# Performance work log

Measured on AMD Instinct MI355X. Metric: run time of the kernel, lower is better.

Reference implementation:

```python
import jax, jax.numpy as jnp
import numpy as np

N_NODES = 500_000
N_EDGES = 16_000_000


def setup_inputs() -> dict:
    key = jax.random.key(0)
    ks = jax.random.split(key, 10)
    x = jax.random.normal(ks[0], (N_NODES, 8), dtype=jnp.float32)
    edge_index = jax.random.randint(ks[1], (2, N_EDGES), 0, N_NODES, dtype=jnp.int64)
    W1_l = jax.random.normal(ks[2], (8, 32), dtype=jnp.float32) * 0.1
    W1_r = jax.random.normal(ks[3], (8, 32), dtype=jnp.float32) * 0.1
    b1 = jax.random.normal(ks[4], (32,), dtype=jnp.float32) * 0.1
    W2_l = jax.random.normal(ks[5], (32, 16), dtype=jnp.float32) * 0.1
    W2_r = jax.random.normal(ks[6], (32, 16), dtype=jnp.float32) * 0.1
    b2 = jax.random.normal(ks[7], (16,), dtype=jnp.float32) * 0.1
    W_out = jax.random.normal(ks[8], (16, 1), dtype=jnp.float32) * 0.1
    b_out = jax.random.normal(ks[9], (1,), dtype=jnp.float32) * 0.1
    return {"x": x, "edge_index": edge_index, "W1_l": W1_l, "W1_r": W1_r, "b1": b1,
            "W2_l": W2_l, "W2_r": W2_r, "b2": b2, "W_out": W_out, "b_out": b_out}


def _sage_conv(x, src, dst, deg_inv, W_l, W_r, b):
    # mean-aggregate neighbor features: gather x[src], scatter-add to dst, divide by degree
    agg = jax.ops.segment_sum(x[src], dst, num_segments=N_NODES)  # [N, d_in]
    mean_nb = agg * deg_inv[:, None]
    return mean_nb @ W_l + x @ W_r + b


def reference(x, edge_index, W1_l, W1_r, b1, W2_l, W2_r, b2, W_out, b_out):
    src, dst = edge_index[0], edge_index[1]
    # in-degree per target node (mean aggregation denominator), clamped at 1
    deg = jax.ops.segment_sum(jnp.ones((src.shape[0],), dtype=x.dtype), dst,
                              num_segments=N_NODES)
    deg_inv = 1.0 / jnp.maximum(deg, 1.0)
    h = jax.nn.relu(_sage_conv(x, src, dst, deg_inv, W1_l, W1_r, b1))
    # dropout(p=0.1) is identity at inference
    h = jax.nn.relu(_sage_conv(h, src, dst, deg_inv, W2_l, W2_r, b2))
    return jax.nn.sigmoid(h @ W_out + b_out)  # [N, 1]
```

## Files before the change

kernel.cpp:

```cpp
#include <hip/hip_runtime.h>
#include <hip/hip_fp16.h>
#include <math.h>

#define N_NODES 500000
#define N_EDGES 16000000

#define NBUCKET 2048
#define NPB 256
#define NSB 64
#define NSLICE 32
#define NB_USED 1954
#define BUCKET_CAP 9216

#define NCH_H 500
#define CHUNK_H 32000
#define NCH_A 1000
#define CHUNK_A 16000

#define OFF_TOT     0
#define OFF_BASE    8192
#define OFF_FCUR    16512
#define OFF_SBCUR   24704
#define OFF_AUXB    24960
#define OFF_ROW     25600
#define OFF_DEG     2025600
#define OFF_XH8     4025600
#define OFF_PAIRS   8025664
#define OFF_AUX     72025664
#define OFF_H1P8    72025664
#define OFF_S2      80025664

typedef float v2f __attribute__((ext_vector_type(2)));

static __device__ inline float2 up2(unsigned int u) {
  __half2 h = *reinterpret_cast<__half2*>(&u);
  return __half22float2(h);
}
static __device__ inline unsigned int ph2(float a, float b) {
  __half2 h = __floats2half2_rn(a, b);
  return *reinterpret_cast<unsigned int*>(&h);
}
static __device__ inline unsigned int pk_fp8x4(float a, float b, float c, float d) {
  int u = __builtin_amdgcn_cvt_pk_fp8_f32(a, b, 0, false);
  u = __builtin_amdgcn_cvt_pk_fp8_f32(c, d, u, true);
  return (unsigned int)u;
}
static __device__ inline void acc8(float* a, uint2 g) {
  v2f f01 = __builtin_amdgcn_cvt_pk_f32_fp8((int)g.x, false);
  v2f f23 = __builtin_amdgcn_cvt_pk_f32_fp8((int)g.x, true);
  v2f f45 = __builtin_amdgcn_cvt_pk_f32_fp8((int)g.y, false);
  v2f f67 = __builtin_amdgcn_cvt_pk_f32_fp8((int)g.y, true);
  a[0] += f01.x; a[1] += f01.y; a[2] += f23.x; a[3] += f23.y;
  a[4] += f45.x; a[5] += f45.y; a[6] += f67.x; a[7] += f67.y;
}
static __device__ inline void acc16(float* a, uint4 g) {
  v2f f0 = __builtin_amdgcn_cvt_pk_f32_fp8((int)g.x, false);
  v2f f1 = __builtin_amdgcn_cvt_pk_f32_fp8((int)g.x, true);
  v2f f2 = __builtin_amdgcn_cvt_pk_f32_fp8((int)g.y, false);
  v2f f3 = __builtin_amdgcn_cvt_pk_f32_fp8((int)g.y, true);
  v2f f4 = __builtin_amdgcn_cvt_pk_f32_fp8((int)g.z, false);
  v2f f5 = __builtin_amdgcn_cvt_pk_f32_fp8((int)g.z, true);
  v2f f6 = __builtin_amdgcn_cvt_pk_f32_fp8((int)g.w, false);
  v2f f7 = __builtin_amdgcn_cvt_pk_f32_fp8((int)g.w, true);
  a[0] += f0.x;  a[1] += f0.y;  a[2] += f1.x;  a[3] += f1.y;
  a[4] += f2.x;  a[5] += f2.y;  a[6] += f3.x;  a[7] += f3.y;
  a[8] += f4.x;  a[9] += f4.y;  a[10] += f5.x; a[11] += f5.y;
  a[12] += f6.x; a[13] += f6.y; a[14] += f7.x; a[15] += f7.y;
}

__global__ __launch_bounds__(256) void k_xcast(const float* __restrict__ x,
                                               uint2* __restrict__ xh8) {
  int i = blockIdx.x * 256 + threadIdx.x;
  if (i >= N_NODES) return;
  const float4* xp = (const float4*)(x + (size_t)i * 8);
  float4 a = xp[0], b = xp[1];
  uint2 v;
  v.x = pk_fp8x4(a.x, a.y, a.z, a.w);
  v.y = pk_fp8x4(b.x, b.y, b.z, b.w);
  xh8[i] = v;
}

__global__ __launch_bounds__(256) void k_hist(const int* __restrict__ ei,
                                              int* __restrict__ tot) {
  __shared__ int hist[NBUCKET];
  int t = threadIdx.x;
  int c = blockIdx.x;
#pragma unroll
  for (int j = 0; j < NBUCKET / 256; j++) hist[t + j * 256] = 0;
  __syncthreads();
  int e0 = c * CHUNK_H;
  const int ng = CHUNK_H / 4;
  for (int g = t; g < ng; g += 256) {
    uint4 d4 = *(const uint4*)(ei + N_EDGES + e0 + g * 4);
    atomicAdd(&hist[d4.x >> 8], 1);
    atomicAdd(&hist[d4.y >> 8], 1);
    atomicAdd(&hist[d4.z >> 8], 1);
    atomicAdd(&hist[d4.w >> 8], 1);
  }
  __syncthreads();
#pragma unroll
  for (int j = 0; j < NBUCKET / 256; j++) {
    int b = t + j * 256;
    if (hist[b]) atomicAdd(&tot[b], hist[b]);
  }
}

__global__ __launch_bounds__(256) void k_scan(const int* __restrict__ tot,
                                              int* __restrict__ base,
                                              int* __restrict__ fineCur,
                                              int* __restrict__ sbCur,
                                              int* __restrict__ auxBase) {
  __shared__ int lds[256];
  int t = threadIdx.x;
  int loc[8];
  int s = 0;
#pragma unroll
  for (int j = 0; j < 8; j++) {
    loc[j] = s;
    s += tot[t * 8 + j];
  }
  lds[t] = s;
  __syncthreads();
  for (int off = 1; off < 256; off <<= 1) {
    int v = (t >= off) ? lds[t - off] : 0;
    __syncthreads();
    lds[t] += v;
    __syncthreads();
  }
  int eb = (t > 0) ? lds[t - 1] : 0;
#pragma unroll
  for (int j = 0; j < 8; j++) {
    int idx = t * 8 + j;
    int v = eb + loc[j];
    base[idx] = v;
    fineCur[idx] = v;
  }
  if (t == 255) base[NBUCKET] = lds[255];
  if (t < NSB) {
    int v = (t > 0) ? lds[t * 4 - 1] : 0;
    if (t >= 32) v -= lds[127];
    sbCur[t] = v;
    auxBase[t] = v;
  }
}

__global__ __launch_bounds__(256) void k_passA(const int* __restrict__ ei,
                                               int* __restrict__ sbCur,
                                               unsigned int* __restrict__ aux,
                                               int half) {
  __shared__ int hist[NSB];
  __shared__ int cur[NSB];
  int t = threadIdx.x;
  int c = blockIdx.x;
  if (t < NSB) hist[t] = 0;
  __syncthreads();
  int e0 = c * CHUNK_A;
  const int ng = CHUNK_A / 4;
  for (int g = t; g < ng; g += 256) {
    uint4 d4 = *(const uint4*)(ei + N_EDGES + e0 + g * 4);
    unsigned int dd[4] = {d4.x, d4.y, d4.z, d4.w};
#pragma unroll
    for (int j = 0; j < 4; j++) {
      int sb = (int)(dd[j] >> 13);
      if ((sb >> 5) == half) atomicAdd(&hist[sb], 1);
    }
  }
  __syncthreads();
  if (t < NSB) cur[t] = atomicAdd(&sbCur[t], hist[t]);
  __syncthreads();
  for (int g = t; g < ng; g += 256) {
    uint4 s4 = *(const uint4*)(ei + e0 + g * 4);
    uint4 d4 = *(const uint4*)(ei + N_EDGES + e0 + g * 4);
    unsigned int ss[4] = {s4.x, s4.y, s4.z, s4.w};
    unsigned int dd[4] = {d4.x, d4.y, d4.z, d4.w};
#pragma unroll
    for (int j = 0; j < 4; j++) {
      int sb = (int)(dd[j] >> 13);
      if ((sb >> 5) == half) {
        int pos = atomicAdd(&cur[sb], 1);
        aux[pos] = ss[j] | ((dd[j] & 8191u) << 19);
      }
    }
  }
}

__global__ __launch_bounds__(256) void k_passB(const unsigned int* __restrict__ aux,
                                               const int* __restrict__ base,
                                               const int* __restrict__ auxBase,
                                               int* __restrict__ fineCur,
                                               unsigned int* __restrict__ pairs,
                                               int half) {
  __shared__ int hist[32];
  __shared__ int cur[32];
  int t = threadIdx.x;
  int sbl = blockIdx.x / NSLICE;
  int sl = blockIdx.x % NSLICE;
  int sb = half * 32 + sbl;
  int aStart = auxBase[sb];
  int len = base[(sb + 1) << 5] - base[sb << 5];
  int per = (len + NSLICE - 1) / NSLICE;
  int lo = sl * per;
  int hi = lo + per;
  if (hi > len) hi = len;
  if (t < 32) hist[t] = 0;
  __syncthreads();
  for (int k = lo + t; k < hi; k += 256) {
    unsigned int w = aux[aStart + k];
    atomicAdd(&hist[w >> 27], 1);
  }
  __syncthreads();
  if (t < 32) cur[t] = atomicAdd(&fineCur[(sb << 5) + t], hist[t]);
  __syncthreads();
  for (int k = lo + t; k < hi; k += 256) {
    unsigned int w = aux[aStart + k];
    int pos = atomicAdd(&cur[w >> 27], 1);
    pairs[pos] = w;
  }
}

__global__ __launch_bounds__(256) void k_sort(unsigned int* __restrict__ pairs,
                                              const int* __restrict__ base,
                                              int* __restrict__ row,
                                              int* __restrict__ deg) {
  __shared__ unsigned int sp[BUCKET_CAP];
  __shared__ int hist[NPB];
  __shared__ int lds[NPB];
  __shared__ int cur[NPB];
  int t = threadIdx.x;
  int b = blockIdx.x;
  int e0 = base[b];
  int n = base[b + 1] - e0;
  if (n > BUCKET_CAP) n = BUCKET_CAP;
  for (int k = t; k < n; k += 256) sp[k] = pairs[e0 + k];
  hist[t] = 0;
  __syncthreads();
  for (int k = t; k < n; k += 256) atomicAdd(&hist[(sp[k] >> 19) & 255u], 1);
  __syncthreads();
  int h = hist[t];
  lds[t] = h;
  __syncthreads();
  for (int off = 1; off < 256; off <<= 1) {
    int v = (t >= off) ? lds[t - off] : 0;
    __syncthreads();
    lds[t] += v;
    __syncthreads();
  }
  int start = e0 + lds[t] - h;
  cur[t] = start;
  int i = (b << 8) + t;
  if (i < N_NODES) {
    row[i] = start;
    deg[i] = h;
  }
  __syncthreads();
  for (int k = t; k < n; k += 256) {
    unsigned int p = sp[k];
    int ld = (int)((p >> 19) & 255u);
    int pos = atomicAdd(&cur[ld], 1);
    pairs[pos] = p & 0x7FFFFu;
  }
}

__global__ __launch_bounds__(256) void k_l1(
    const unsigned int* __restrict__ adj, const int* __restrict__ row,
    const int* __restrict__ deg, const uint2* __restrict__ xh8,
    const float* __restrict__ x,
    const float* __restrict__ W1l, const float* __restrict__ W1r,
    const float* __restrict__ b1,
    const float* __restrict__ W2l, const float* __restrict__ W2r,
    uint4* __restrict__ h1p8, unsigned int* __restrict__ s2) {
  __shared__ float sW1l[256], sW1r[256], sb1[32], sW2l[512], sW2r[512];
  int t = threadIdx.x;
  sW1l[t] = W1l[t];
  sW1r[t] = W1r[t];
  sW2l[t] = W2l[t];  sW2l[t + 256] = W2l[t + 256];
  sW2r[t] = W2r[t];  sW2r[t + 256] = W2r[t + 256];
  if (t < 32) sb1[t] = b1[t];
  __syncthreads();

  int i = blockIdx.x * 256 + t;
  if (i >= N_NODES) return;
  int rs = row[i];
  int d = deg[i];

  float acc[8] = {0, 0, 0, 0, 0, 0, 0, 0};
  int j = 0;
  for (; j + 4 <= d; j += 4) {
    int a0 = adj[rs + j + 0];
    int a1 = adj[rs + j + 1];
    int a2 = adj[rs + j + 2];
    int a3 = adj[rs + j + 3];
    uint2 g0 = xh8[a0], g1 = xh8[a1], g2 = xh8[a2], g3 = xh8[a3];
    acc8(acc, g0); acc8(acc, g1); acc8(acc, g2); acc8(acc, g3);
  }
  for (; j < d; j++) {
    uint2 g = xh8[adj[rs + j]];
    acc8(acc, g);
  }

  float dinv = 1.0f / fmaxf((float)d, 1.0f);
  float m[8];
#pragma unroll
  for (int f = 0; f < 8; f++) m[f] = acc[f] * dinv;
  const float4* xp = (const float4*)(x + (size_t)i * 8);
  float4 x0 = xp[0], x1 = xp[1];
  float xv[8] = {x0.x, x0.y, x0.z, x0.w, x1.x, x1.y, x1.z, x1.w};

  float h[32];
#pragma unroll
  for (int jj = 0; jj < 32; jj++) h[jj] = sb1[jj];
#pragma unroll
  for (int k = 0; k < 8; k++) {
#pragma unroll
    for (int jj = 0; jj < 32; jj++) {
      h[jj] = fmaf(m[k], sW1l[k * 32 + jj], h[jj]);
      h[jj] = fmaf(xv[k], sW1r[k * 32 + jj], h[jj]);
    }
  }
#pragma unroll
  for (int jj = 0; jj < 32; jj++) h[jj] = fmaxf(h[jj], 0.0f);

  float p[16], s[16];
#pragma unroll
  for (int jj = 0; jj < 16; jj++) { p[jj] = 0.0f; s[jj] = 0.0f; }
#pragma unroll
  for (int k = 0; k < 32; k++) {
#pragma unroll
    for (int jj = 0; jj < 16; jj++) {
      p[jj] = fmaf(h[k], sW2l[k * 16 + jj], p[jj]);
      s[jj] = fmaf(h[k], sW2r[k * 16 + jj], s[jj]);
    }
  }
  uint4 hv;
  hv.x = pk_fp8x4(p[0], p[1], p[2], p[3]);
  hv.y = pk_fp8x4(p[4], p[5], p[6], p[7]);
  hv.z = pk_fp8x4(p[8], p[9], p[10], p[11]);
  hv.w = pk_fp8x4(p[12], p[13], p[14], p[15]);
  h1p8[i] = hv;
  uint4* sp = (uint4*)(s2 + (size_t)i * 8);
  sp[0] = make_uint4(ph2(s[0], s[1]), ph2(s[2], s[3]), ph2(s[4], s[5]), ph2(s[6], s[7]));
  sp[1] = make_uint4(ph2(s[8], s[9]), ph2(s[10], s[11]), ph2(s[12], s[13]), ph2(s[14], s[15]));
}

__global__ __launch_bounds__(256) void k_l2(
    const unsigned int* __restrict__ adj, const int* __restrict__ row,
    const int* __restrict__ deg, const uint4* __restrict__ h1p8,
    const unsigned int* __restrict__ s2, const float* __restrict__ b2,
    const float* __restrict__ Wout, const float* __restrict__ bout,
    float* __restrict__ out) {
  __shared__ float sb2[16], sWo[16], sbo;
  int t = threadIdx.x;
  if (t < 16) { sb2[t] = b2[t]; sWo[t] = Wout[t]; }
  if (t == 0) sbo = bout[0];
  __syncthreads();

  int i = blockIdx.x * 256 + t;
  if (i >= N_NODES) return;
  int rs = row[i];
  int d = deg[i];

  float acc[16];
#pragma unroll
  for (int jj = 0; jj < 16; jj++) acc[jj] = 0.0f;
  int j = 0;
  for (; j + 4 <= d; j += 4) {
    int a0 = adj[rs + j + 0];
    int a1 = adj[rs + j + 1];
    int a2 = adj[rs + j + 2];
    int a3 = adj[rs + j + 3];
    uint4 g0 = h1p8[a0], g1 = h1p8[a1], g2 = h1p8[a2], g3 = h1p8[a3];
    acc16(acc, g0); acc16(acc, g1); acc16(acc, g2); acc16(acc, g3);
  }
  for (; j < d; j++) {
    uint4 g = h1p8[adj[rs + j]];
    acc16(acc, g);
  }

  float dinv = 1.0f / fmaxf((float)d, 1.0f);
  const uint4* sp = (const uint4*)(s2 + (size_t)i * 8);
  uint4 q0 = sp[0], q1 = sp[1];
  float2 s0 = up2(q0.x), s1 = up2(q0.y), s2v = up2(q0.z), s3 = up2(q0.w);
  float2 s4 = up2(q1.x), s5 = up2(q1.y), s6 = up2(q1.z), s7 = up2(q1.w);
  float sv[16] = {s0.x, s0.y, s1.x, s1.y, s2v.x, s2v.y, s3.x, s3.y,
                  s4.x, s4.y, s5.x, s5.y, s6.x, s6.y, s7.x, s7.y};
  float o = sbo;
#pragma unroll
  for (int c = 0; c < 16; c++) {
    float h2 = fmaxf(acc[c] * dinv + sv[c] + sb2[c], 0.0f);
    o = fmaf(h2, sWo[c], o);
  }
  out[i] = 1.0f / (1.0f + expf(-o));
}

extern "C" void kernel_launch(void* const* d_in, const int* in_sizes, int n_in,
                              void* d_out, int out_size, void* d_ws, size_t ws_size,
                              hipStream_t stream) {
  const float* x    = (const float*)d_in[0];
  const int*   ei   = (const int*)d_in[1];
  const float* W1l  = (const float*)d_in[2];
  const float* W1r  = (const float*)d_in[3];
  const float* b1   = (const float*)d_in[4];
  const float* W2l  = (const float*)d_in[5];
  const float* W2r  = (const float*)d_in[6];
  const float* b2   = (const float*)d_in[7];
  const float* Wout = (const float*)d_in[8];
  const float* bout = (const float*)d_in[9];
  float* out = (float*)d_out;

  char* ws = (char*)d_ws;
  int* tot     = (int*)(ws + OFF_TOT);
  int* base    = (int*)(ws + OFF_BASE);
  int* fineCur = (int*)(ws + OFF_FCUR);
  int* sbCur   = (int*)(ws + OFF_SBCUR);
  int* auxBase = (int*)(ws + OFF_AUXB);
  int* row     = (int*)(ws + OFF_ROW);
  int* deg     = (int*)(ws + OFF_DEG);
  uint2* xh8   = (uint2*)(ws + OFF_XH8);
  unsigned int* pairs = (unsigned int*)(ws + OFF_PAIRS);
  unsigned int* aux   = (unsigned int*)(ws + OFF_AUX);
  uint4* h1p8  = (uint4*)(ws + OFF_H1P8);
  unsigned int* s2 = (unsigned int*)(ws + OFF_S2);

  hipMemsetAsync(tot, 0, NBUCKET * sizeof(int), stream);

  k_xcast<<<NB_USED, 256, 0, stream>>>(x, xh8);
  k_hist<<<NCH_H, 256, 0, stream>>>(ei, tot);
  k_scan<<<1, 256, 0, stream>>>(tot, base, fineCur, sbCur, auxBase);
  k_passA<<<NCH_A, 256, 0, stream>>>(ei, sbCur, aux, 0);
  k_passB<<<32 * NSLICE, 256, 0, stream>>>(aux, base, auxBase, fineCur, pairs, 0);
  k_passA<<<NCH_A, 256, 0, stream>>>(ei, sbCur, aux, 1);
  k_passB<<<32 * NSLICE, 256, 0, stream>>>(aux, base, auxBase, fineCur, pairs, 1);
  k_sort<<<NBUCKET, 256, 0, stream>>>(pairs, base, row, deg);
  k_l1<<<NB_USED, 256, 0, stream>>>(pairs, row, deg, xh8, x, W1l, W1r, b1,
                                    W2l, W2r, h1p8, s2);
  k_l2<<<NB_USED, 256, 0, stream>>>(pairs, row, deg, h1p8, s2, b2, Wout,
                                    bout, out);
}
```

Measured before the change: 902.2 us.

## Split layer-2 gather into two half-feature passes with nontemporal adjacency loads

Layer-1 output is now written as two separate 8-byte fp8 halves (channels 0-7 and 8-15), plus matching fp16 self-term halves. The layer-2 gather runs as two passes over the adjacency, each touching only an 8-byte-per-node table, so the random-gather working set (4 MB per half) fits better in cache. A partial output buffer carries the first half's contribution to the second pass, which applies the sigmoid. Adjacency and streaming buffers use nontemporal loads and stores to avoid polluting cache, at the cost of reading the adjacency list twice in layer 2.

```diff
diff --git a/kernel.cpp b/kernel.cpp
--- a/kernel.cpp
+++ b/kernel.cpp
@@ -27,10 +27,14 @@
 #define OFF_XH8     4025600
 #define OFF_PAIRS   8025664
 #define OFF_AUX     72025664
-#define OFF_H1P8    72025664
-#define OFF_S2      80025664
+#define OFF_H1LO    72025664
+#define OFF_H1HI    76025664
+#define OFF_S2LO    80025664
+#define OFF_S2HI    88025664
+#define OFF_PO      96025664
 
 typedef float v2f __attribute__((ext_vector_type(2)));
+typedef unsigned int v4u __attribute__((ext_vector_type(4)));
 
 static __device__ inline float2 up2(unsigned int u) {
   __half2 h = *reinterpret_cast<__half2*>(&u);
@@ -52,20 +56,6 @@
   v2f f67 = __builtin_amdgcn_cvt_pk_f32_fp8((int)g.y, true);
   a[0] += f01.x; a[1] += f01.y; a[2] += f23.x; a[3] += f23.y;
   a[4] += f45.x; a[5] += f45.y; a[6] += f67.x; a[7] += f67.y;
-}
-static __device__ inline void acc16(float* a, uint4 g) {
-  v2f f0 = __builtin_amdgcn_cvt_pk_f32_fp8((int)g.x, false);
-  v2f f1 = __builtin_amdgcn_cvt_pk_f32_fp8((int)g.x, true);
-  v2f f2 = __builtin_amdgcn_cvt_pk_f32_fp8((int)g.y, false);
-  v2f f3 = __builtin_amdgcn_cvt_pk_f32_fp8((int)g.y, true);
-  v2f f4 = __builtin_amdgcn_cvt_pk_f32_fp8((int)g.z, false);
-  v2f f5 = __builtin_amdgcn_cvt_pk_f32_fp8((int)g.z, true);
-  v2f f6 = __builtin_amdgcn_cvt_pk_f32_fp8((int)g.w, false);
-  v2f f7 = __builtin_amdgcn_cvt_pk_f32_fp8((int)g.w, true);
-  a[0] += f0.x;  a[1] += f0.y;  a[2] += f1.x;  a[3] += f1.y;
-  a[4] += f2.x;  a[5] += f2.y;  a[6] += f3.x;  a[7] += f3.y;
-  a[8] += f4.x;  a[9] += f4.y;  a[10] += f5.x; a[11] += f5.y;
-  a[12] += f6.x; a[13] += f6.y; a[14] += f7.x; a[15] += f7.y;
 }
 
 __global__ __launch_bounds__(256) void k_xcast(const float* __restrict__ x,
@@ -268,7 +258,8 @@
     const float* __restrict__ W1l, const float* __restrict__ W1r,
     const float* __restrict__ b1,
     const float* __restrict__ W2l, const float* __restrict__ W2r,
-    uint4* __restrict__ h1p8, unsigned int* __restrict__ s2) {
+    uint2* __restrict__ h1lo, uint2* __restrict__ h1hi,
+    v4u* __restrict__ s2lo, v4u* __restrict__ s2hi) {
   __shared__ float sW1l[256], sW1r[256], sb1[32], sW2l[512], sW2r[512];
   int t = threadIdx.x;
   sW1l[t] = W1l[t];
@@ -286,15 +277,15 @@
   float acc[8] = {0, 0, 0, 0, 0, 0, 0, 0};
   int j = 0;
   for (; j + 4 <= d; j += 4) {
-    int a0 = adj[rs + j + 0];
-    int a1 = adj[rs + j + 1];
-    int a2 = adj[rs + j + 2];
-    int a3 = adj[rs + j + 3];
+    int a0 = (int)__builtin_nontemporal_load(&adj[rs + j + 0]);
+    int a1 = (int)__builtin_nontemporal_load(&adj[rs + j + 1]);
+    int a2 = (int)__builtin_nontemporal_load(&adj[rs + j + 2]);
+    int a3 = (int)__builtin_nontemporal_load(&adj[rs + j + 3]);
     uint2 g0 = xh8[a0], g1 = xh8[a1], g2 = xh8[a2], g3 = xh8[a3];
     acc8(acc, g0); acc8(acc, g1); acc8(acc, g2); acc8(acc, g3);
   }
   for (; j < d; j++) {
-    uint2 g = xh8[adj[rs + j]];
+    uint2 g = xh8[(int)__builtin_nontemporal_load(&adj[rs + j])];
     acc8(acc, g);
   }
 
@@ -331,26 +322,31 @@
       s[jj] = fmaf(h[k], sW2r[k * 16 + jj], s[jj]);
     }
   }
-  uint4 hv;
-  hv.x = pk_fp8x4(p[0], p[1], p[2], p[3]);
-  hv.y = pk_fp8x4(p[4], p[5], p[6], p[7]);
-  hv.z = pk_fp8x4(p[8], p[9], p[10], p[11]);
-  hv.w = pk_fp8x4(p[12], p[13], p[14], p[15]);
-  h1p8[i] = hv;
-  uint4* sp = (uint4*)(s2 + (size_t)i * 8);
-  sp[0] = make_uint4(ph2(s[0], s[1]), ph2(s[2], s[3]), ph2(s[4], s[5]), ph2(s[6], s[7]));
-  sp[1] = make_uint4(ph2(s[8], s[9]), ph2(s[10], s[11]), ph2(s[12], s[13]), ph2(s[14], s[15]));
-}
-
-__global__ __launch_bounds__(256) void k_l2(
+  uint2 lo, hi;
+  lo.x = pk_fp8x4(p[0], p[1], p[2], p[3]);
+  lo.y = pk_fp8x4(p[4], p[5], p[6], p[7]);
+  hi.x = pk_fp8x4(p[8], p[9], p[10], p[11]);
+  hi.y = pk_fp8x4(p[12], p[13], p[14], p[15]);
+  h1lo[i] = lo;
+  h1hi[i] = hi;
+  v4u slo, shi;
+  slo.x = ph2(s[0], s[1]);  slo.y = ph2(s[2], s[3]);
+  slo.z = ph2(s[4], s[5]);  slo.w = ph2(s[6], s[7]);
+  shi.x = ph2(s[8], s[9]);  shi.y = ph2(s[10], s[11]);
+  shi.z = ph2(s[12], s[13]); shi.w = ph2(s[14], s[15]);
+  __builtin_nontemporal_store(slo, &s2lo[i]);
+  __builtin_nontemporal_store(shi, &s2hi[i]);
+}
+
+__global__ __launch_bounds__(256) void k_l2h(
     const unsigned int* __restrict__ adj, const int* __restrict__ row,
-    const int* __restrict__ deg, const uint4* __restrict__ h1p8,
-    const unsigned int* __restrict__ s2, const float* __restrict__ b2,
-    const float* __restrict__ Wout, const float* __restrict__ bout,
-    float* __restrict__ out) {
-  __shared__ float sb2[16], sWo[16], sbo;
-  int t = threadIdx.x;
-  if (t < 16) { sb2[t] = b2[t]; sWo[t] = Wout[t]; }
+    const int* __restrict__ deg, const uint2* __restrict__ h1,
+    const v4u* __restrict__ s2h, const float* __restrict__ b2h,
+    const float* __restrict__ Woh, const float* __restrict__ bout,
+    float* __restrict__ po, float* __restrict__ out, int phase) {
+  __shared__ float sb2[8], sWo[8], sbo;
+  int t = threadIdx.x;
+  if (t < 8) { sb2[t] = b2h[t]; sWo[t] = Woh[t]; }
   if (t == 0) sbo = bout[0];
   __syncthreads();
 
@@ -359,37 +355,37 @@
   int rs = row[i];
   int d = deg[i];
 
-  float acc[16];
-#pragma unroll
-  for (int jj = 0; jj < 16; jj++) acc[jj] = 0.0f;
+  float acc[8] = {0, 0, 0, 0, 0, 0, 0, 0};
   int j = 0;
   for (; j + 4 <= d; j += 4) {
-    int a0 = adj[rs + j + 0];
-    int a1 = adj[rs + j + 1];
-    int a2 = adj[rs + j + 2];
-    int a3 = adj[rs + j + 3];
-    uint4 g0 = h1p8[a0], g1 = h1p8[a1], g2 = h1p8[a2], g3 = h1p8[a3];
-    acc16(acc, g0); acc16(acc, g1); acc16(acc, g2); acc16(acc, g3);
+    int a0 = (int)__builtin_nontemporal_load(&adj[rs + j + 0]);
+    int a1 = (int)__builtin_nontemporal_load(&adj[rs + j + 1]);
+    int a2 = (int)__builtin_nontemporal_load(&adj[rs + j + 2]);
+    int a3 = (int)__builtin_nontemporal_load(&adj[rs + j + 3]);
+    uint2 g0 = h1[a0], g1 = h1[a1], g2 = h1[a2], g3 = h1[a3];
+    acc8(acc, g0); acc8(acc, g1); acc8(acc, g2); acc8(acc, g3);
   }
   for (; j < d; j++) {
-    uint4 g = h1p8[adj[rs + j]];
-    acc16(acc, g);
+    uint2 g = h1[(int)__builtin_nontemporal_load(&adj[rs + j])];
+    acc8(acc, g);
   }
 
   float dinv = 1.0f / fmaxf((float)d, 1.0f);
-  const uint4* sp = (const uint4*)(s2 + (size_t)i * 8);
-  uint4 q0 = sp[0], q1 = sp[1];
-  float2 s0 = up2(q0.x), s1 = up2(q0.y), s2v = up2(q0.z), s3 = up2(q0.w);
-  float2 s4 = up2(q1.x), s5 = up2(q1.y), s6 = up2(q1.z), s7 = up2(q1.w);
-  float sv[16] = {s0.x, s0.y, s1.x, s1.y, s2v.x, s2v.y, s3.x, s3.y,
-                  s4.x, s4.y, s5.x, s5.y, s6.x, s6.y, s7.x, s7.y};
-  float o = sbo;
-#pragma unroll
-  for (int c = 0; c < 16; c++) {
+  v4u q = __builtin_nontemporal_load(&s2h[i]);
+  float2 s0 = up2(q.x), s1 = up2(q.y), s2v = up2(q.z), s3 = up2(q.w);
+  float sv[8] = {s0.x, s0.y, s1.x, s1.y, s2v.x, s2v.y, s3.x, s3.y};
+  float o = 0.0f;
+#pragma unroll
+  for (int c = 0; c < 8; c++) {
     float h2 = fmaxf(acc[c] * dinv + sv[c] + sb2[c], 0.0f);
     o = fmaf(h2, sWo[c], o);
   }
-  out[i] = 1.0f / (1.0f + expf(-o));
+  if (phase == 0) {
+    __builtin_nontemporal_store(o, &po[i]);
+  } else {
+    float z = __builtin_nontemporal_load(&po[i]) + o + sbo;
+    out[i] = 1.0f / (1.0f + expf(-z));
+  }
 }
 
 extern "C" void kernel_launch(void* const* d_in, const int* in_sizes, int n_in,
@@ -418,10 +414,13 @@
   uint2* xh8   = (uint2*)(ws + OFF_XH8);
   unsigned int* pairs = (unsigned int*)(ws + OFF_PAIRS);
   unsigned int* aux   = (unsigned int*)(ws + OFF_AUX);
-  uint4* h1p8  = (uint4*)(ws + OFF_H1P8);
-  unsigned int* s2 = (unsigned int*)(ws + OFF_S2);
-
-  hipMemsetAsync(tot, 0, NBUCKET * sizeof(int), stream);
+  uint2* h1lo  = (uint2*)(ws + OFF_H1LO);
+  uint2* h1hi  = (uint2*)(ws + OFF_H1HI);
+  v4u* s2lo    = (v4u*)(ws + OFF_S2LO);
+  v4u* s2hi    = (v4u*)(ws + OFF_S2HI);
+  float* po    = (float*)(ws + OFF_PO);
+
+  (void)hipMemsetAsync(tot, 0, NBUCKET * sizeof(int), stream);
 
   k_xcast<<<NB_USED, 256, 0, stream>>>(x, xh8);
   k_hist<<<NCH_H, 256, 0, stream>>>(ei, tot);
@@ -432,7 +431,9 @@
   k_passB<<<32 * NSLICE, 256, 0, stream>>>(aux, base, auxBase, fineCur, pairs, 1);
   k_sort<<<NBUCKET, 256, 0, stream>>>(pairs, base, row, deg);
   k_l1<<<NB_USED, 256, 0, stream>>>(pairs, row, deg, xh8, x, W1l, W1r, b1,
-                                    W2l, W2r, h1p8, s2);
-  k_l2<<<NB_USED, 256, 0, stream>>>(pairs, row, deg, h1p8, s2, b2, Wout,
-                                    bout, out);
-}
+                                    W2l, W2r, h1lo, h1hi, s2lo, s2hi);
+  k_l2h<<<NB_USED, 256, 0, stream>>>(pairs, row, deg, h1lo, s2lo, b2, Wout,
+                                     bout, po, out, 0);
+  k_l2h<<<NB_USED, 256, 0, stream>>>(pairs, row, deg, h1hi, s2hi, b2 + 8,
+                                     Wout + 8, bout, po, out, 1);
+}
```

Result: slower. 977.1 us (+8.3%).

## Sub-sort each node's neighbors by source quarter and add nontemporal hints

Applied to the files above, without the earlier changes.

The per-bucket sort now keys on destination node plus the top two bits of the source index, so each node's adjacency list is grouped into four source-range quarters. Per-quarter counts are packed into a new degq array, and the aggregation kernels walk the quarters in order. This gives the gather over xh8 and h1p8 more locality in time across the wavefront. Adjacency, s2 and h1p8 accesses also use nontemporal loads and stores so they pollute the cache less. In exchange the sort uses larger LDS histograms, and the per-quarter loops add remainder overhead. The packing assumes each quarter holds fewer than 256 neighbors.

```diff
diff --git a/kernel.cpp b/kernel.cpp
--- a/kernel.cpp
+++ b/kernel.cpp
@@ -29,8 +29,10 @@
 #define OFF_AUX     72025664
 #define OFF_H1P8    72025664
 #define OFF_S2      80025664
+#define OFF_DEGQ    96025664
 
 typedef float v2f __attribute__((ext_vector_type(2)));
+typedef unsigned int v4u __attribute__((ext_vector_type(4)));
 
 static __device__ inline float2 up2(unsigned int u) {
   __half2 h = *reinterpret_cast<__half2*>(&u);
@@ -221,23 +223,30 @@
 __global__ __launch_bounds__(256) void k_sort(unsigned int* __restrict__ pairs,
                                               const int* __restrict__ base,
                                               int* __restrict__ row,
-                                              int* __restrict__ deg) {
+                                              int* __restrict__ deg,
+                                              unsigned int* __restrict__ degq) {
   __shared__ unsigned int sp[BUCKET_CAP];
-  __shared__ int hist[NPB];
-  __shared__ int lds[NPB];
-  __shared__ int cur[NPB];
+  __shared__ int hist[1024];
+  __shared__ int cur[1024];
+  __shared__ int lds[256];
   int t = threadIdx.x;
   int b = blockIdx.x;
   int e0 = base[b];
   int n = base[b + 1] - e0;
   if (n > BUCKET_CAP) n = BUCKET_CAP;
   for (int k = t; k < n; k += 256) sp[k] = pairs[e0 + k];
-  hist[t] = 0;
-  __syncthreads();
-  for (int k = t; k < n; k += 256) atomicAdd(&hist[(sp[k] >> 19) & 255u], 1);
-  __syncthreads();
-  int h = hist[t];
-  lds[t] = h;
+#pragma unroll
+  for (int j = 0; j < 4; j++) hist[t + j * 256] = 0;
+  __syncthreads();
+  for (int k = t; k < n; k += 256) {
+    unsigned int p = sp[k];
+    int key = (int)(((p >> 19) & 255u) << 2) | (int)((p & 0x7FFFFu) >> 17);
+    atomicAdd(&hist[key], 1);
+  }
+  __syncthreads();
+  int h0 = hist[4 * t], h1 = hist[4 * t + 1], h2 = hist[4 * t + 2], h3 = hist[4 * t + 3];
+  int s = h0 + h1 + h2 + h3;
+  lds[t] = s;
   __syncthreads();
   for (int off = 1; off < 256; off <<= 1) {
     int v = (t >= off) ? lds[t - off] : 0;
@@ -245,30 +254,35 @@
     lds[t] += v;
     __syncthreads();
   }
-  int start = e0 + lds[t] - h;
-  cur[t] = start;
+  int ebase = (t > 0) ? lds[t - 1] : 0;
+  cur[4 * t] = e0 + ebase;
+  cur[4 * t + 1] = e0 + ebase + h0;
+  cur[4 * t + 2] = e0 + ebase + h0 + h1;
+  cur[4 * t + 3] = e0 + ebase + h0 + h1 + h2;
   int i = (b << 8) + t;
   if (i < N_NODES) {
-    row[i] = start;
-    deg[i] = h;
+    row[i] = e0 + ebase;
+    deg[i] = s;
+    degq[i] = (unsigned)h0 | ((unsigned)h1 << 8) | ((unsigned)h2 << 16) |
+              ((unsigned)h3 << 24);
   }
   __syncthreads();
   for (int k = t; k < n; k += 256) {
     unsigned int p = sp[k];
-    int ld = (int)((p >> 19) & 255u);
-    int pos = atomicAdd(&cur[ld], 1);
+    int key = (int)(((p >> 19) & 255u) << 2) | (int)((p & 0x7FFFFu) >> 17);
+    int pos = atomicAdd(&cur[key], 1);
     pairs[pos] = p & 0x7FFFFu;
   }
 }
 
 __global__ __launch_bounds__(256) void k_l1(
     const unsigned int* __restrict__ adj, const int* __restrict__ row,
-    const int* __restrict__ deg, const uint2* __restrict__ xh8,
+    const unsigned int* __restrict__ degq, const uint2* __restrict__ xh8,
     const float* __restrict__ x,
     const float* __restrict__ W1l, const float* __restrict__ W1r,
     const float* __restrict__ b1,
     const float* __restrict__ W2l, const float* __restrict__ W2r,
-    uint4* __restrict__ h1p8, unsigned int* __restrict__ s2) {
+    v4u* __restrict__ h1p8, v4u* __restrict__ s2) {
   __shared__ float sW1l[256], sW1r[256], sb1[32], sW2l[512], sW2r[512];
   int t = threadIdx.x;
   sW1l[t] = W1l[t];
@@ -281,21 +295,29 @@
   int i = blockIdx.x * 256 + t;
   if (i >= N_NODES) return;
   int rs = row[i];
-  int d = deg[i];
+  unsigned dq = degq[i];
+  int d = (int)((dq & 255u) + ((dq >> 8) & 255u) + ((dq >> 16) & 255u) + (dq >> 24));
 
   float acc[8] = {0, 0, 0, 0, 0, 0, 0, 0};
-  int j = 0;
-  for (; j + 4 <= d; j += 4) {
-    int a0 = adj[rs + j + 0];
-    int a1 = adj[rs + j + 1];
-    int a2 = adj[rs + j + 2];
-    int a3 = adj[rs + j + 3];
-    uint2 g0 = xh8[a0], g1 = xh8[a1], g2 = xh8[a2], g3 = xh8[a3];
-    acc8(acc, g0); acc8(acc, g1); acc8(acc, g2); acc8(acc, g3);
-  }
-  for (; j < d; j++) {
-    uint2 g = xh8[adj[rs + j]];
-    acc8(acc, g);
+  int off = 0;
+#pragma unroll
+  for (int q = 0; q < 4; q++) {
+    int len = (int)((dq >> (8 * q)) & 255u);
+    int js = rs + off;
+    int j = 0;
+    for (; j + 4 <= len; j += 4) {
+      int a0 = (int)__builtin_nontemporal_load(&adj[js + j + 0]);
+      int a1 = (int)__builtin_nontemporal_load(&adj[js + j + 1]);
+      int a2 = (int)__builtin_nontemporal_load(&adj[js + j + 2]);
+      int a3 = (int)__builtin_nontemporal_load(&adj[js + j + 3]);
+      uint2 g0 = xh8[a0], g1 = xh8[a1], g2 = xh8[a2], g3 = xh8[a3];
+      acc8(acc, g0); acc8(acc, g1); acc8(acc, g2); acc8(acc, g3);
+    }
+    for (; j < len; j++) {
+      uint2 g = xh8[(int)__builtin_nontemporal_load(&adj[js + j])];
+      acc8(acc, g);
+    }
+    off += len;
   }
 
   float dinv = 1.0f / fmaxf((float)d, 1.0f);
@@ -331,21 +353,25 @@
       s[jj] = fmaf(h[k], sW2r[k * 16 + jj], s[jj]);
     }
   }
-  uint4 hv;
+  v4u hv;
   hv.x = pk_fp8x4(p[0], p[1], p[2], p[3]);
   hv.y = pk_fp8x4(p[4], p[5], p[6], p[7]);
   hv.z = pk_fp8x4(p[8], p[9], p[10], p[11]);
   hv.w = pk_fp8x4(p[12], p[13], p[14], p[15]);
-  h1p8[i] = hv;
-  uint4* sp = (uint4*)(s2 + (size_t)i * 8);
-  sp[0] = make_uint4(ph2(s[0], s[1]), ph2(s[2], s[3]), ph2(s[4], s[5]), ph2(s[6], s[7]));
-  sp[1] = make_uint4(ph2(s[8], s[9]), ph2(s[10], s[11]), ph2(s[12], s[13]), ph2(s[14], s[15]));
+  __builtin_nontemporal_store(hv, &h1p8[i]);
+  v4u slo, shi;
+  slo.x = ph2(s[0], s[1]);   slo.y = ph2(s[2], s[3]);
+  slo.z = ph2(s[4], s[5]);   slo.w = ph2(s[6], s[7]);
+  shi.x = ph2(s[8], s[9]);   shi.y = ph2(s[10], s[11]);
+  shi.z = ph2(s[12], s[13]); shi.w = ph2(s[14], s[15]);
+  __builtin_nontemporal_store(slo, &s2[(size_t)i * 2]);
+  __builtin_nontemporal_store(shi, &s2[(size_t)i * 2 + 1]);
 }
 
 __global__ __launch_bounds__(256) void k_l2(
     const unsigned int* __restrict__ adj, const int* __restrict__ row,
-    const int* __restrict__ deg, const uint4* __restrict__ h1p8,
-    const unsigned int* __restrict__ s2, const float* __restrict__ b2,
+    const unsigned int* __restrict__ degq, const uint4* __restrict__ h1p8,
+    const v4u* __restrict__ s2, const float* __restrict__ b2,
     const float* __restrict__ Wout, const float* __restrict__ bout,
     float* __restrict__ out) {
   __shared__ float sb2[16], sWo[16], sbo;
@@ -357,28 +383,36 @@
   int i = blockIdx.x * 256 + t;
   if (i >= N_NODES) return;
   int rs = row[i];
-  int d = deg[i];
+  unsigned dq = degq[i];
+  int d = (int)((dq & 255u) + ((dq >> 8) & 255u) + ((dq >> 16) & 255u) + (dq >> 24));
 
   float acc[16];
 #pragma unroll
   for (int jj = 0; jj < 16; jj++) acc[jj] = 0.0f;
-  int j = 0;
-  for (; j + 4 <= d; j += 4) {
-    int a0 = adj[rs + j + 0];
-    int a1 = adj[rs + j + 1];
-    int a2 = adj[rs + j + 2];
-    int a3 = adj[rs + j + 3];
-    uint4 g0 = h1p8[a0], g1 = h1p8[a1], g2 = h1p8[a2], g3 = h1p8[a3];
-    acc16(acc, g0); acc16(acc, g1); acc16(acc, g2); acc16(acc, g3);
-  }
-  for (; j < d; j++) {
-    uint4 g = h1p8[adj[rs + j]];
-    acc16(acc, g);
+  int off = 0;
+#pragma unroll
+  for (int q = 0; q < 4; q++) {
+    int len = (int)((dq >> (8 * q)) & 255u);
+    int js = rs + off;
+    int j = 0;
+    for (; j + 4 <= len; j += 4) {
+      int a0 = (int)__builtin_nontemporal_load(&adj[js + j + 0]);
+      int a1 = (int)__builtin_nontemporal_load(&adj[js + j + 1]);
+      int a2 = (int)__builtin_nontemporal_load(&adj[js + j + 2]);
+      int a3 = (int)__builtin_nontemporal_load(&adj[js + j + 3]);
+      uint4 g0 = h1p8[a0], g1 = h1p8[a1], g2 = h1p8[a2], g3 = h1p8[a3];
+      acc16(acc, g0); acc16(acc, g1); acc16(acc, g2); acc16(acc, g3);
+    }
+    for (; j < len; j++) {
+      uint4 g = h1p8[(int)__builtin_nontemporal_load(&adj[js + j])];
+      acc16(acc, g);
+    }
+    off += len;
   }
 
   float dinv = 1.0f / fmaxf((float)d, 1.0f);
-  const uint4* sp = (const uint4*)(s2 + (size_t)i * 8);
-  uint4 q0 = sp[0], q1 = sp[1];
+  v4u q0 = __builtin_nontemporal_load(&s2[(size_t)i * 2]);
+  v4u q1 = __builtin_nontemporal_load(&s2[(size_t)i * 2 + 1]);
   float2 s0 = up2(q0.x), s1 = up2(q0.y), s2v = up2(q0.z), s3 = up2(q0.w);
   float2 s4 = up2(q1.x), s5 = up2(q1.y), s6 = up2(q1.z), s7 = up2(q1.w);
   float sv[16] = {s0.x, s0.y, s1.x, s1.y, s2v.x, s2v.y, s3.x, s3.y,
@@ -418,10 +452,11 @@
   uint2* xh8   = (uint2*)(ws + OFF_XH8);
   unsigned int* pairs = (unsigned int*)(ws + OFF_PAIRS);
   unsigned int* aux   = (unsigned int*)(ws + OFF_AUX);
-  uint4* h1p8  = (uint4*)(ws + OFF_H1P8);
-  unsigned int* s2 = (unsigned int*)(ws + OFF_S2);
-
-  hipMemsetAsync(tot, 0, NBUCKET * sizeof(int), stream);
+  v4u* h1p8    = (v4u*)(ws + OFF_H1P8);
+  v4u* s2      = (v4u*)(ws + OFF_S2);
+  unsigned int* degq = (unsigned int*)(ws + OFF_DEGQ);
+
+  (void)hipMemsetAsync(tot, 0, NBUCKET * sizeof(int), stream);
 
   k_xcast<<<NB_USED, 256, 0, stream>>>(x, xh8);
   k_hist<<<NCH_H, 256, 0, stream>>>(ei, tot);
@@ -430,9 +465,9 @@
   k_passB<<<32 * NSLICE, 256, 0, stream>>>(aux, base, auxBase, fineCur, pairs, 0);
   k_passA<<<NCH_A, 256, 0, stream>>>(ei, sbCur, aux, 1);
   k_passB<<<32 * NSLICE, 256, 0, stream>>>(aux, base, auxBase, fineCur, pairs, 1);
-  k_sort<<<NBUCKET, 256, 0, stream>>>(pairs, base, row, deg);
-  k_l1<<<NB_USED, 256, 0, stream>>>(pairs, row, deg, xh8, x, W1l, W1r, b1,
+  k_sort<<<NBUCKET, 256, 0, stream>>>(pairs, base, row, deg, degq);
+  k_l1<<<NB_USED, 256, 0, stream>>>(pairs, row, degq, xh8, x, W1l, W1r, b1,
                                     W2l, W2r, h1p8, s2);
-  k_l2<<<NB_USED, 256, 0, stream>>>(pairs, row, deg, h1p8, s2, b2, Wout,
-                                    bout, out);
-}
+  k_l2<<<NB_USED, 256, 0, stream>>>(pairs, row, degq, (const uint4*)h1p8, s2,
+                                    b2, Wout, bout, out);
+}
```

After: 880.8 us. 2.4% less time.
